# Optimization experiments

Hardware: AMD Instinct MI355X
Metric: run time of the kernel (lower is better)

Reference implementation:

```python
import jax, jax.numpy as jnp
import numpy as np

DIM_IN = 1024
DIM_OUT = 1024
NUM_HEADS = 16
HEAD_DIM = DIM_OUT // NUM_HEADS


def setup_inputs() -> dict:
    key = jax.random.key(0)
    k1, k2, k3, k4 = jax.random.split(key, 4)
    X = jax.random.normal(k1, (4, 2048, DIM_IN), dtype=jnp.float32)
    W_qkv = jax.random.normal(k2, (DIM_IN, 3 * DIM_OUT), dtype=jnp.float32) * (DIM_IN ** -0.5)
    W_out = jax.random.normal(k3, (DIM_OUT, DIM_OUT), dtype=jnp.float32) * (DIM_OUT ** -0.5)
    b_out = jax.random.normal(k4, (DIM_OUT,), dtype=jnp.float32) * 0.01
    return {"X": X, "W_qkv": W_qkv, "W_out": W_out, "b_out": b_out}


def reference(X, W_qkv, W_out, b_out):
    B, S, _ = X.shape
    qkv = X @ W_qkv  # [B, S, 3*dim_out]
    qkv = qkv.reshape(B, S, 3, NUM_HEADS, HEAD_DIM).transpose(2, 0, 3, 1, 4)
    q, k, v = qkv[0], qkv[1], qkv[2]  # each [B, H, S, hd]
    scores = jnp.einsum('bhqd,bhkd->bhqk', q, k)  # [B, H, S, S]
    causal = jnp.triu(jnp.ones((S, S), dtype=bool), k=1)
    scores = jnp.where(causal, -jnp.inf, scores)
    attn = jax.nn.softmax(scores * (HEAD_DIM ** -0.5), axis=-1)
    ctx = jnp.einsum('bhqk,bhkd->bhqd', attn, v)  # [B, H, S, hd]
    ctx = ctx.transpose(0, 2, 1, 3).reshape(B, S, DIM_OUT)
    return ctx @ W_out + b_out
```

## Files before the change

### kernel.cpp

```cpp
#include <hip/hip_runtime.h>
#include <hip/hip_bf16.h>

typedef __bf16 bf16_t;
typedef __bf16 bf16x8 __attribute__((ext_vector_type(8)));
typedef __bf16 bf16x4 __attribute__((ext_vector_type(4)));
typedef float f32x4 __attribute__((ext_vector_type(4)));

#define AS1(p) ((const __attribute__((address_space(1))) void*)(p))
#define AS3(p) ((__attribute__((address_space(3))) void*)(p))

#define QSCALE 0.1803368801111204f

__global__ void cast_x_kernel(const float* __restrict__ X, bf16_t* __restrict__ Xb) {
  int i = (blockIdx.x * 256 + threadIdx.x) * 4;
  float4 v = *(const float4*)(X + i);
  bf16x4 o;
  o[0] = (bf16_t)v.x; o[1] = (bf16_t)v.y; o[2] = (bf16_t)v.z; o[3] = (bf16_t)v.w;
  *(bf16x4*)(Xb + i) = o;
}

__global__ void transpose_cast_kernel(const float* __restrict__ W, bf16_t* __restrict__ Wt,
                                      int K, int N) {
  __shared__ float tile[32][33];
  int n0 = blockIdx.x * 32, k0 = blockIdx.y * 32;
  int tx = threadIdx.x, ty = threadIdx.y;
  for (int r = ty; r < 32; r += 8)
    tile[r][tx] = W[(size_t)(k0 + r) * N + n0 + tx];
  __syncthreads();
  for (int r = ty; r < 32; r += 8)
    Wt[(size_t)(n0 + r) * K + k0 + tx] = (bf16_t)tile[tx][r];
}

__global__ __launch_bounds__(256) void gemm_qkv_kernel(
    const bf16_t* __restrict__ A, const bf16_t* __restrict__ Bt,
    bf16_t* __restrict__ Qb, bf16_t* __restrict__ Kb, bf16_t* __restrict__ Vt) {
  __shared__ __align__(16) bf16_t As[128 * 32];
  __shared__ __align__(16) bf16_t Bs[128 * 32];
  const int tid = threadIdx.x;
  const int lane = tid & 63, wave = tid >> 6;
  const int quad = lane >> 4, l15 = lane & 15;
  const int wr = wave >> 1, wc = wave & 1;
  const int m0 = blockIdx.x * 128, n0 = blockIdx.y * 128;
  f32x4 acc[4][4];
  const f32x4 vzero = {0.f, 0.f, 0.f, 0.f};
#pragma unroll
  for (int i = 0; i < 4; i++)
#pragma unroll
    for (int j = 0; j < 4; j++) acc[i][j] = vzero;

  for (int kb = 0; kb < 1024; kb += 32) {
    __syncthreads();
#pragma unroll
    for (int i = 0; i < 2; i++) {
      int c = i * 256 + tid;
      int row = c >> 2, kc = c & 3;
      __builtin_amdgcn_global_load_lds(AS1(A + (size_t)(m0 + row) * 1024 + kb + kc * 8),
                                       AS3(As + c * 8), 16, 0, 0);
    }
#pragma unroll
    for (int i = 0; i < 2; i++) {
      int c = i * 256 + tid;
      int row = c >> 2, kc = c & 3;
      __builtin_amdgcn_global_load_lds(AS1(Bt + (size_t)(n0 + row) * 1024 + kb + kc * 8),
                                       AS3(Bs + c * 8), 16, 0, 0);
    }
    __builtin_amdgcn_s_waitcnt(0);
    __syncthreads();
    bf16x8 af[4], bfr[4];
#pragma unroll
    for (int t = 0; t < 4; t++) {
      af[t]  = *(const bf16x8*)(As + (wr * 64 + t * 16 + l15) * 32 + quad * 8);
      bfr[t] = *(const bf16x8*)(Bs + (wc * 64 + t * 16 + l15) * 32 + quad * 8);
    }
#pragma unroll
    for (int mt = 0; mt < 4; mt++)
#pragma unroll
      for (int nt = 0; nt < 4; nt++)
        acc[mt][nt] = __builtin_amdgcn_mfma_f32_16x16x32_bf16(af[mt], bfr[nt], acc[mt][nt], 0, 0, 0);
  }
#pragma unroll
  for (int nt = 0; nt < 4; nt++) {
    int gn = n0 + wc * 64 + nt * 16 + l15;
    int which = gn >> 10;
    int rem = gn & 1023;
    int hh = rem >> 6, dd = rem & 63;
    if (which == 2) {
#pragma unroll
      for (int mt = 0; mt < 4; mt++) {
        int gm0 = m0 + wr * 64 + mt * 16 + quad * 4;
        int b = gm0 >> 11, s = gm0 & 2047;
        bf16x4 o;
#pragma unroll
        for (int r = 0; r < 4; r++) o[r] = (bf16_t)acc[mt][nt][r];
        *(bf16x4*)(Vt + ((size_t)((b << 4) + hh) * 64 + dd) * 2048 + s) = o;
      }
    } else {
      bf16_t* dst = (which == 0) ? Qb : Kb;
      float scl = (which == 0) ? QSCALE : 1.0f;
#pragma unroll
      for (int mt = 0; mt < 4; mt++) {
#pragma unroll
        for (int r = 0; r < 4; r++) {
          int gm = m0 + wr * 64 + mt * 16 + quad * 4 + r;
          int b = gm >> 11, s = gm & 2047;
          dst[((size_t)((b << 4) + hh) * 2048 + s) * 64 + dd] = (bf16_t)(acc[mt][nt][r] * scl);
        }
      }
    }
  }
}

__global__ __launch_bounds__(256, 2) void attn_kernel(
    const bf16_t* __restrict__ Qg_, const bf16_t* __restrict__ Kg_,
    const bf16_t* __restrict__ Vtg_, bf16_t* __restrict__ ctx) {
  __shared__ __align__(16) bf16_t Ks[128 * 72];
  __shared__ __align__(16) bf16_t Vst[64 * 136];
  __shared__ __align__(16) bf16_t Ps[128 * 128];
  const int tid = threadIdx.x;
  const int lane = tid & 63, w = tid >> 6;
  const int quad = lane >> 4, l15 = lane & 15;

  const int bh = blockIdx.x >> 3;
  const int pp = blockIdx.x & 7;
  const int b = bh >> 4, h = bh & 15;
  const size_t base = (size_t)bh * 2048 * 64;
  const bf16_t* Kg = Kg_ + base;
  const bf16_t* Vtg = Vtg_ + base;

  bf16x8 bone;
#pragma unroll
  for (int e = 0; e < 8; e++) bone[e] = (bf16_t)1.0f;

  bf16x8 kr[4], vr[4];
#pragma unroll
  for (int i = 0; i < 4; i++) {
    int c = i * 256 + tid;
    int r = c >> 3, dc = c & 7;
    kr[i] = *(const bf16x8*)(Kg + (size_t)r * 64 + dc * 8);
  }
#pragma unroll
  for (int i = 0; i < 4; i++) {
    int c = i * 256 + tid;
    int r = c >> 4, cc = c & 15;
    vr[i] = *(const bf16x8*)(Vtg + (size_t)r * 2048 + cc * 8);
  }

  const f32x4 vzero = {0.f, 0.f, 0.f, 0.f};

  for (int ti = 0; ti < 2; ti++) {
    const int qb = (ti == 0) ? pp : 15 - pp;
    const int L = qb + 1;

    bf16x8 aq[2][2];
#pragma unroll
    for (int mt = 0; mt < 2; mt++)
#pragma unroll
      for (int ks = 0; ks < 2; ks++)
        aq[mt][ks] = *(const bf16x8*)(Qg_ + base +
                                      (size_t)(qb * 128 + w * 32 + mt * 16 + l15) * 64 +
                                      ks * 32 + quad * 8);

    f32x4 Oacc[2][4], Lacc[2];
#pragma unroll
    for (int mt = 0; mt < 2; mt++) {
#pragma unroll
      for (int dt = 0; dt < 4; dt++) Oacc[mt][dt] = vzero;
      Lacc[mt] = vzero;
    }

    for (int j = 0; j < L; j++) {
      __syncthreads();
#pragma unroll
      for (int i = 0; i < 4; i++) {
        int c = i * 256 + tid;
        int r = c >> 3, dc = c & 7;
        *(bf16x8*)(Ks + r * 72 + dc * 8) = kr[i];
      }
#pragma unroll
      for (int i = 0; i < 4; i++) {
        int c = i * 256 + tid;
        int r = c >> 4, cc = c & 15;
        *(bf16x8*)(Vst + r * 136 + cc * 8) = vr[i];
      }
      __syncthreads();

      const bool havenext = (j + 1 < L) || (ti == 0);
      if (havenext) {
        const int jn = (j + 1 < L) ? j + 1 : 0;
#pragma unroll
        for (int i = 0; i < 4; i++) {
          int c = i * 256 + tid;
          int r = c >> 3, dc = c & 7;
          kr[i] = *(const bf16x8*)(Kg + ((size_t)jn * 128 + r) * 64 + dc * 8);
        }
#pragma unroll
        for (int i = 0; i < 4; i++) {
          int c = i * 256 + tid;
          int r = c >> 4, cc = c & 15;
          vr[i] = *(const bf16x8*)(Vtg + (size_t)r * 2048 + jn * 128 + cc * 8);
        }
      }

      const bool diag = (j == L - 1);

#pragma unroll
      for (int half = 0; half < 2; half++) {
        f32x4 sch[4][2];
#pragma unroll
        for (int nt4 = 0; nt4 < 4; nt4++) {
          const int nt = half * 4 + nt4;
          bf16x8 bk0 = *(const bf16x8*)(Ks + (nt * 16 + l15) * 72 + 0 * 32 + quad * 8);
          bf16x8 bk1 = *(const bf16x8*)(Ks + (nt * 16 + l15) * 72 + 1 * 32 + quad * 8);
#pragma unroll
          for (int mt = 0; mt < 2; mt++) {
            f32x4 s = __builtin_amdgcn_mfma_f32_16x16x32_bf16(aq[mt][0], bk0, vzero, 0, 0, 0);
            sch[nt4][mt] = __builtin_amdgcn_mfma_f32_16x16x32_bf16(aq[mt][1], bk1, s, 0, 0, 0);
          }
        }
#pragma unroll
        for (int nt4 = 0; nt4 < 4; nt4++) {
          const int nt = half * 4 + nt4;
          const int cc = 2 * nt + (l15 >> 3);
          const int pc = (cc ^ (quad << 1)) * 8 + (l15 & 7);
#pragma unroll
          for (int mt = 0; mt < 2; mt++) {
            const int prow = w * 32 + mt * 16 + quad * 4;
#pragma unroll
            for (int r = 0; r < 4; r++) {
              float x = sch[nt4][mt][r];
              if (diag) {
                int kg = (L - 1) * 128 + nt * 16 + l15;
                int qg = qb * 128 + prow + r;
                if (kg > qg) x = -INFINITY;
              }
              Ps[(prow + r) * 128 + pc] = (bf16_t)__builtin_exp2f(x);
            }
          }
        }
      }

#pragma unroll
      for (int ks = 0; ks < 4; ks++) {
        const int pcc = ((ks * 4 + quad) ^ ((l15 >> 2) << 1)) * 8;
        bf16x8 ap[2];
#pragma unroll
        for (int mt = 0; mt < 2; mt++) {
          ap[mt] = *(const bf16x8*)(Ps + (w * 32 + mt * 16 + l15) * 128 + pcc);
          Lacc[mt] = __builtin_amdgcn_mfma_f32_16x16x32_bf16(ap[mt], bone, Lacc[mt], 0, 0, 0);
        }
#pragma unroll
        for (int dt = 0; dt < 4; dt++) {
          bf16x8 bv = *(const bf16x8*)(Vst + (dt * 16 + l15) * 136 + ks * 32 + quad * 8);
#pragma unroll
          for (int mt = 0; mt < 2; mt++)
            Oacc[mt][dt] = __builtin_amdgcn_mfma_f32_16x16x32_bf16(ap[mt], bv, Oacc[mt][dt], 0, 0, 0);
        }
      }
    }

#pragma unroll
    for (int mt = 0; mt < 2; mt++) {
      float rl[4];
#pragma unroll
      for (int r = 0; r < 4; r++) rl[r] = __builtin_amdgcn_rcpf(Lacc[mt][r]);
#pragma unroll
      for (int dt = 0; dt < 4; dt++)
#pragma unroll
        for (int r = 0; r < 4; r++) {
          int qg = qb * 128 + w * 32 + mt * 16 + quad * 4 + r;
          ctx[((size_t)b * 2048 + qg) * 1024 + h * 64 + dt * 16 + l15] =
              (bf16_t)(Oacc[mt][dt][r] * rl[r]);
        }
    }
  }
}

__global__ __launch_bounds__(256) void gemm_out_kernel(
    const bf16_t* __restrict__ A, const bf16_t* __restrict__ Bt,
    const float* __restrict__ bias, float* __restrict__ out) {
  __shared__ __align__(16) bf16_t As[128 * 32];
  __shared__ __align__(16) bf16_t Bs[128 * 32];
  const int tid = threadIdx.x;
  const int lane = tid & 63, wave = tid >> 6;
  const int quad = lane >> 4, l15 = lane & 15;
  const int wr = wave >> 1, wc = wave & 1;
  const int m0 = blockIdx.x * 128, n0 = blockIdx.y * 128;
  f32x4 acc[4][4];
  const f32x4 vzero = {0.f, 0.f, 0.f, 0.f};
#pragma unroll
  for (int i = 0; i < 4; i++)
#pragma unroll
    for (int j = 0; j < 4; j++) acc[i][j] = vzero;

  for (int kb = 0; kb < 1024; kb += 32) {
    __syncthreads();
#pragma unroll
    for (int i = 0; i < 2; i++) {
      int c = i * 256 + tid;
      int row = c >> 2, kc = c & 3;
      __builtin_amdgcn_global_load_lds(AS1(A + (size_t)(m0 + row) * 1024 + kb + kc * 8),
                                       AS3(As + c * 8), 16, 0, 0);
    }
#pragma unroll
    for (int i = 0; i < 2; i++) {
      int c = i * 256 + tid;
      int row = c >> 2, kc = c & 3;
      __builtin_amdgcn_global_load_lds(AS1(Bt + (size_t)(n0 + row) * 1024 + kb + kc * 8),
                                       AS3(Bs + c * 8), 16, 0, 0);
    }
    __builtin_amdgcn_s_waitcnt(0);
    __syncthreads();
    bf16x8 af[4], bfr[4];
#pragma unroll
    for (int t = 0; t < 4; t++) {
      af[t]  = *(const bf16x8*)(As + (wr * 64 + t * 16 + l15) * 32 + quad * 8);
      bfr[t] = *(const bf16x8*)(Bs + (wc * 64 + t * 16 + l15) * 32 + quad * 8);
    }
#pragma unroll
    for (int mt = 0; mt < 4; mt++)
#pragma unroll
      for (int nt = 0; nt < 4; nt++)
        acc[mt][nt] = __builtin_amdgcn_mfma_f32_16x16x32_bf16(af[mt], bfr[nt], acc[mt][nt], 0, 0, 0);
  }
#pragma unroll
  for (int nt = 0; nt < 4; nt++) {
    int gn = n0 + wc * 64 + nt * 16 + l15;
    float bv = bias[gn];
#pragma unroll
    for (int mt = 0; mt < 4; mt++) {
#pragma unroll
      for (int r = 0; r < 4; r++) {
        int gm = m0 + wr * 64 + mt * 16 + quad * 4 + r;
        out[(size_t)gm * 1024 + gn] = acc[mt][nt][r] + bv;
      }
    }
  }
}

extern "C" void kernel_launch(void* const* d_in, const int* in_sizes, int n_in,
                              void* d_out, int out_size, void* d_ws, size_t ws_size,
                              hipStream_t stream) {
  (void)in_sizes; (void)n_in; (void)out_size; (void)ws_size;
  const float* X     = (const float*)d_in[0];
  const float* W_qkv = (const float*)d_in[1];
  const float* W_out = (const float*)d_in[2];
  const float* b_out = (const float*)d_in[3];
  float* out = (float*)d_out;

  char* ws = (char*)d_ws;
  bf16_t* Xb    = (bf16_t*)(ws);
  bf16_t* Wqkvt = (bf16_t*)(ws + 16777216);
  bf16_t* Woutt = (bf16_t*)(ws + 23068672);
  bf16_t* Qb    = (bf16_t*)(ws + 25165824);
  bf16_t* Kb    = (bf16_t*)(ws + 41943040);
  bf16_t* Vt    = (bf16_t*)(ws + 58720256);
  bf16_t* ctx   = (bf16_t*)(ws + 75497472);

  cast_x_kernel<<<8192, 256, 0, stream>>>(X, Xb);
  transpose_cast_kernel<<<dim3(96, 32), dim3(32, 8), 0, stream>>>(W_qkv, Wqkvt, 1024, 3072);
  transpose_cast_kernel<<<dim3(32, 32), dim3(32, 8), 0, stream>>>(W_out, Woutt, 1024, 1024);
  gemm_qkv_kernel<<<dim3(64, 24), 256, 0, stream>>>(Xb, Wqkvt, Qb, Kb, Vt);
  attn_kernel<<<dim3(512), 256, 0, stream>>>(Qb, Kb, Vt, ctx);
  gemm_out_kernel<<<dim3(64, 8), 256, 0, stream>>>(ctx, Woutt, b_out, out);
}
```

Before: 272.8 us.

## Keep attention probabilities in registers, drop LDS P buffer and MFMA row-sum

Computes S transposed (K as the A operand) so each lane's score fragment already matches the A-operand layout of the PV MFMA, with K rows permuted when staged into shared memory. The probabilities go straight from registers into the PV MFMA, which removes the Ps shared buffer, its store/load round trip and the ones-vector MFMA used for the row sum. Row sums are now accumulated in scalars and reduced with cross-lane shuffles at the end. The freed shared memory allows raising launch bounds to 3 blocks per CU, which may add register pressure.

```diff
diff --git a/kernel.cpp b/kernel.cpp
--- a/kernel.cpp
+++ b/kernel.cpp
@@ -110,12 +110,11 @@
   }
 }
 
-__global__ __launch_bounds__(256, 2) void attn_kernel(
+__global__ __launch_bounds__(256, 3) void attn_kernel(
     const bf16_t* __restrict__ Qg_, const bf16_t* __restrict__ Kg_,
     const bf16_t* __restrict__ Vtg_, bf16_t* __restrict__ ctx) {
   __shared__ __align__(16) bf16_t Ks[128 * 72];
   __shared__ __align__(16) bf16_t Vst[64 * 136];
-  __shared__ __align__(16) bf16_t Ps[128 * 128];
   const int tid = threadIdx.x;
   const int lane = tid & 63, w = tid >> 6;
   const int quad = lane >> 4, l15 = lane & 15;
@@ -127,10 +126,6 @@
   const bf16_t* Kg = Kg_ + base;
   const bf16_t* Vtg = Vtg_ + base;
 
-  bf16x8 bone;
-#pragma unroll
-  for (int e = 0; e < 8; e++) bone[e] = (bf16_t)1.0f;
-
   bf16x8 kr[4], vr[4];
 #pragma unroll
   for (int i = 0; i < 4; i++) {
@@ -160,12 +155,13 @@
                                       (size_t)(qb * 128 + w * 32 + mt * 16 + l15) * 64 +
                                       ks * 32 + quad * 8);
 
-    f32x4 Oacc[2][4], Lacc[2];
+    f32x4 Oacc[2][4];
+    float rsum[2];
 #pragma unroll
     for (int mt = 0; mt < 2; mt++) {
 #pragma unroll
       for (int dt = 0; dt < 4; dt++) Oacc[mt][dt] = vzero;
-      Lacc[mt] = vzero;
+      rsum[mt] = 0.f;
     }
 
     for (int j = 0; j < L; j++) {
@@ -173,8 +169,9 @@
 #pragma unroll
       for (int i = 0; i < 4; i++) {
         int c = i * 256 + tid;
-        int r = c >> 3, dc = c & 7;
-        *(bf16x8*)(Ks + r * 72 + dc * 8) = kr[i];
+        int k = c >> 3, dc = c & 7;
+        int kp = (k & 0x60) | ((k & 4) << 2) | ((k & 0x18) >> 1) | (k & 3);
+        *(bf16x8*)(Ks + kp * 72 + dc * 8) = kr[i];
       }
 #pragma unroll
       for (int i = 0; i < 4; i++) {
@@ -204,65 +201,55 @@
       const bool diag = (j == L - 1);
 
 #pragma unroll
-      for (int half = 0; half < 2; half++) {
-        f32x4 sch[4][2];
-#pragma unroll
-        for (int nt4 = 0; nt4 < 4; nt4++) {
-          const int nt = half * 4 + nt4;
-          bf16x8 bk0 = *(const bf16x8*)(Ks + (nt * 16 + l15) * 72 + 0 * 32 + quad * 8);
-          bf16x8 bk1 = *(const bf16x8*)(Ks + (nt * 16 + l15) * 72 + 1 * 32 + quad * 8);
+      for (int g = 0; g < 4; g++) {
+        f32x4 sch[2][2];
+#pragma unroll
+        for (int bs = 0; bs < 2; bs++) {
+          const int nt = 2 * g + bs;
+          bf16x8 bk0 = *(const bf16x8*)(Ks + (nt * 16 + l15) * 72 + quad * 8);
+          bf16x8 bk1 = *(const bf16x8*)(Ks + (nt * 16 + l15) * 72 + 32 + quad * 8);
 #pragma unroll
           for (int mt = 0; mt < 2; mt++) {
-            f32x4 s = __builtin_amdgcn_mfma_f32_16x16x32_bf16(aq[mt][0], bk0, vzero, 0, 0, 0);
-            sch[nt4][mt] = __builtin_amdgcn_mfma_f32_16x16x32_bf16(aq[mt][1], bk1, s, 0, 0, 0);
+            f32x4 s0 = __builtin_amdgcn_mfma_f32_16x16x32_bf16(bk0, aq[mt][0], vzero, 0, 0, 0);
+            sch[bs][mt] = __builtin_amdgcn_mfma_f32_16x16x32_bf16(bk1, aq[mt][1], s0, 0, 0, 0);
           }
         }
-#pragma unroll
-        for (int nt4 = 0; nt4 < 4; nt4++) {
-          const int nt = half * 4 + nt4;
-          const int cc = 2 * nt + (l15 >> 3);
-          const int pc = (cc ^ (quad << 1)) * 8 + (l15 & 7);
-#pragma unroll
-          for (int mt = 0; mt < 2; mt++) {
-            const int prow = w * 32 + mt * 16 + quad * 4;
+        bf16x8 pfrag[2];
+#pragma unroll
+        for (int mt = 0; mt < 2; mt++) {
+          const int qg_ = qb * 128 + w * 32 + mt * 16 + l15;
+#pragma unroll
+          for (int bs = 0; bs < 2; bs++) {
+            const int kb_ = j * 128 + g * 32 + quad * 8 + bs * 4;
 #pragma unroll
             for (int r = 0; r < 4; r++) {
-              float x = sch[nt4][mt][r];
-              if (diag) {
-                int kg = (L - 1) * 128 + nt * 16 + l15;
-                int qg = qb * 128 + prow + r;
-                if (kg > qg) x = -INFINITY;
-              }
-              Ps[(prow + r) * 128 + pc] = (bf16_t)__builtin_exp2f(x);
+              float x = sch[bs][mt][r];
+              if (diag && (kb_ + r > qg_)) x = -INFINITY;
+              float p = __builtin_exp2f(x);
+              rsum[mt] += p;
+              pfrag[mt][bs * 4 + r] = (bf16_t)p;
             }
           }
         }
-      }
-
-#pragma unroll
-      for (int ks = 0; ks < 4; ks++) {
-        const int pcc = ((ks * 4 + quad) ^ ((l15 >> 2) << 1)) * 8;
-        bf16x8 ap[2];
-#pragma unroll
-        for (int mt = 0; mt < 2; mt++) {
-          ap[mt] = *(const bf16x8*)(Ps + (w * 32 + mt * 16 + l15) * 128 + pcc);
-          Lacc[mt] = __builtin_amdgcn_mfma_f32_16x16x32_bf16(ap[mt], bone, Lacc[mt], 0, 0, 0);
-        }
 #pragma unroll
         for (int dt = 0; dt < 4; dt++) {
-          bf16x8 bv = *(const bf16x8*)(Vst + (dt * 16 + l15) * 136 + ks * 32 + quad * 8);
+          bf16x8 bv = *(const bf16x8*)(Vst + (dt * 16 + l15) * 136 + g * 32 + quad * 8);
 #pragma unroll
           for (int mt = 0; mt < 2; mt++)
-            Oacc[mt][dt] = __builtin_amdgcn_mfma_f32_16x16x32_bf16(ap[mt], bv, Oacc[mt][dt], 0, 0, 0);
+            Oacc[mt][dt] = __builtin_amdgcn_mfma_f32_16x16x32_bf16(pfrag[mt], bv, Oacc[mt][dt], 0, 0, 0);
         }
       }
     }
 
 #pragma unroll
     for (int mt = 0; mt < 2; mt++) {
+      float s = rsum[mt];
+      s += __shfl_xor(s, 16);
+      s += __shfl_xor(s, 32);
       float rl[4];
 #pragma unroll
-      for (int r = 0; r < 4; r++) rl[r] = __builtin_amdgcn_rcpf(Lacc[mt][r]);
+      for (int r = 0; r < 4; r++)
+        rl[r] = __builtin_amdgcn_rcpf(__shfl(s, quad * 4 + r));
 #pragma unroll
       for (int dt = 0; dt < 4; dt++)
 #pragma unroll
```

After: 274.7 us. About the same (+0.7%).
